# Kernel optimization log

Measured on AMD Instinct MI355X. Metric: run time of the kernel, lower is better.

Reference implementation:

```python
import jax, jax.numpy as jnp
import numpy as np

N = 16384       # num_nodes
IN = 128        # in_features
OUT = 128       # out_features
E = 524288      # num edges
NG = 8          # FastKAN num_grids
GRID_MIN, GRID_MAX = -2.0, 2.0
LN_EPS = 1e-5


def setup_inputs() -> dict:
    key = jax.random.key(0)
    ks = jax.random.split(key, 6)
    x = jax.random.normal(ks[0], (N, IN), dtype=jnp.float32)
    edge_index = jax.random.randint(ks[1], (2, E), 0, N, dtype=jnp.int32)
    # FastKANLayer params
    ln_gamma = jnp.ones((IN,), jnp.float32)
    ln_beta = jnp.zeros((IN,), jnp.float32)
    # SplineLinear: trunc-normal-ish init with scale 0.1 (fast-kan default)
    spline_w = (jax.random.normal(ks[2], (OUT, IN * NG), jnp.float32)
                * (0.1 / np.sqrt(IN * NG)))
    base_w = jax.random.normal(ks[3], (OUT, IN), jnp.float32) / np.sqrt(IN)
    base_b = jnp.zeros((OUT,), jnp.float32)
    # GCNConv.bias
    bias = jax.random.normal(ks[4], (OUT,), jnp.float32) * 0.01
    return dict(x=x, edge_index=edge_index, ln_gamma=ln_gamma, ln_beta=ln_beta,
                spline_w=spline_w, base_w=base_w, base_b=base_b, bias=bias)


def _fastkan(x, ln_gamma, ln_beta, spline_w, base_w, base_b):
    # LayerNorm
    mu = jnp.mean(x, axis=-1, keepdims=True)
    var = jnp.mean((x - mu) ** 2, axis=-1, keepdims=True)
    h = (x - mu) * jax.lax.rsqrt(var + LN_EPS) * ln_gamma + ln_beta
    # Gaussian RBF basis over fixed grid
    grid = jnp.linspace(GRID_MIN, GRID_MAX, NG)
    denom = (GRID_MAX - GRID_MIN) / (NG - 1)
    basis = jnp.exp(-(((h[..., None] - grid) / denom) ** 2))  # [N, IN, NG]
    out = basis.reshape(x.shape[0], IN * NG) @ spline_w.T      # [N, OUT]
    out = out + jax.nn.silu(x) @ base_w.T + base_b             # base update
    return out


def reference(x, edge_index, ln_gamma, ln_beta, spline_w, base_w, base_b, bias):
    num_nodes = x.shape[0]
    # Dense symmetric adjacency, exactly as the torch module builds it
    adj = jnp.zeros((num_nodes, num_nodes), x.dtype)
    adj = adj.at[edge_index[0], edge_index[1]].set(1.0)
    adj = adj.at[edge_index[1], edge_index[0]].set(1.0)
    deg = jnp.sum(adj, axis=1)
    dis = 1.0 / jnp.sqrt(deg)
    norm_adj = adj * dis[:, None] * dis[None, :]
    support = _fastkan(x, ln_gamma, ln_beta, spline_w, base_w, base_b)
    return norm_adj @ support + bias
```

## Files before the change

kernel.cpp:

```cpp
#include <hip/hip_runtime.h>

#define N_NODES 16384
#define NE 524288
#define KDIM 1152
#define KPH 576
#define KPAD2 584
#define KSTEPS_PH 18
#define NBUCK 1024
#define SBLK 512
#define SPB 2048
#define MROW 516
#define DCAP 256

typedef unsigned int uint32;
typedef unsigned short ushort;
typedef __attribute__((ext_vector_type(8))) short bf16x8;
typedef __attribute__((ext_vector_type(4))) float f32x4;

__device__ __forceinline__ ushort f2bf(float f) {
    unsigned u = __float_as_uint(f);
    unsigned r = (u + 0x7fffu + ((u >> 16) & 1u)) >> 16;
    return (ushort)r;
}
__device__ __forceinline__ float bflo(uint32 u) {
    return __uint_as_float(u << 16);
}
__device__ __forceinline__ float bfhi(uint32 u) {
    return __uint_as_float(u & 0xffff0000u);
}

__global__ __launch_bounds__(256) void pre_kernel(
    const int* __restrict__ ei, uint32* __restrict__ ebuf,
    uint32* __restrict__ ocnt, const float* __restrict__ sw,
    const float* __restrict__ bw, ushort* __restrict__ Wp) {
    const int t = threadIdx.x;
    if (blockIdx.x >= SBLK) {
        int idx = (blockIdx.x - SBLK) * 256 + t;
        int i  = idx & 7;
        int l  = (idx >> 3) & 63;
        int ct = (idx >> 9) & 7;
        int kk = idx >> 12;
        int kp  = kk * 32 + ((l >> 4) << 3) + i;
        int p   = kp / KPH;
        int r   = kp - p * KPH;
        int col = ct * 16 + (l & 15);
        float v;
        if (r < 512) {
            int ch = p * 64 + (r >> 3);
            int g  = r & 7;
            v = sw[col * 1024 + ch * 8 + g];
        } else {
            int ch = p * 64 + (r - 512);
            v = bw[col * 128 + ch];
        }
        Wp[idx] = f2bf(v);
        return;
    }
    __shared__ int hcnt[NBUCK];
    __shared__ int lbase[NBUCK];
    __shared__ int ps[256];
    __shared__ uint32 st[SPB];
    for (int q = t; q < NBUCK; q += 256) hcnt[q] = 0;
    __syncthreads();

    int bk[8], sl[8];
    uint32 pk[8];
#pragma unroll
    for (int k = 0; k < 4; ++k) {
        int e = blockIdx.x * 1024 + k * 256 + t;
        int a = ei[e];
        int b = ei[NE + e];
        bk[2 * k]     = a >> 4;
        pk[2 * k]     = ((uint32)(a & 15) << 14) | (uint32)b;
        bk[2 * k + 1] = b >> 4;
        pk[2 * k + 1] = ((uint32)(b & 15) << 14) | (uint32)a;
        sl[2 * k]     = atomicAdd(&hcnt[bk[2 * k]], 1);
        sl[2 * k + 1] = atomicAdd(&hcnt[bk[2 * k + 1]], 1);
    }
    __syncthreads();

    int c[4], loc[4];
    int s = 0;
#pragma unroll
    for (int q = 0; q < 4; ++q) {
        c[q] = hcnt[t * 4 + q];
        loc[q] = s;
        s += c[q];
    }
    ps[t] = s;
    __syncthreads();
    for (int off = 1; off < 256; off <<= 1) {
        int v = ps[t];
        int add = (t >= off) ? ps[t - off] : 0;
        __syncthreads();
        ps[t] = v + add;
        __syncthreads();
    }
    const int base = (t == 0) ? 0 : ps[t - 1];
    uint32* oc = ocnt + (size_t)blockIdx.x * NBUCK;
#pragma unroll
    for (int q = 0; q < 4; ++q) {
        int e0 = base + loc[q];
        lbase[t * 4 + q] = e0;
        oc[t * 4 + q] = (uint32)e0 | ((uint32)c[q] << 16);
    }
    __syncthreads();

#pragma unroll
    for (int k = 0; k < 8; ++k) st[lbase[bk[k]] + sl[k]] = pk[k];
    __syncthreads();
    uint32* gout = ebuf + (size_t)blockIdx.x * SPB;
#pragma unroll
    for (int k = 0; k < 8; ++k) gout[t + k * 256] = st[t + k * 256];
}

__global__ __launch_bounds__(256) void mid_kernel(
    const uint32* __restrict__ ebuf, const uint32* __restrict__ ocnt,
    float* __restrict__ dis, int* __restrict__ degarr,
    ushort* __restrict__ dadj, const float* __restrict__ x,
    const float* __restrict__ gamma, const float* __restrict__ beta,
    const ushort* __restrict__ Wp, const float* __restrict__ base_b,
    ushort* __restrict__ S) {
    __shared__ __align__(16) ushort smem[32 * KPAD2];
    const int t = threadIdx.x;
    const int lane = t & 63;
    const int w = t >> 6;
    const int role = blockIdx.x % 3;

    if (role < 2) {
        uint32* mask = (uint32*)smem;
        const int bkt = (blockIdx.x / 3) * 2 + role;
        for (int i = t; i < 16 * MROW; i += 256) mask[i] = 0;
        __syncthreads();

        const uint32 oc0 = ocnt[(size_t)t * NBUCK + bkt];
        const uint32 oc1 = ocnt[(size_t)(t + 256) * NBUCK + bkt];
#pragma unroll
        for (int h = 0; h < 2; ++h) {
            const int b = h ? (t + 256) : t;
            const uint32 oc = h ? oc1 : oc0;
            int off = (int)(oc & 0xFFFFu);
            int cn  = (int)(oc >> 16);
            const uint32* p = ebuf + (size_t)b * SPB + off;
            for (int s = 0; s < cn; ++s) {
                uint32 e = p[s];
                atomicOr(&mask[(e >> 14) * MROW + ((e & 16383) >> 5)],
                         1u << (e & 31));
            }
        }
        __syncthreads();

        for (int n = w * 4; n < w * 4 + 4; ++n) {
            const uint32* row = &mask[n * MROW];
            uint32 wd[8];
            int c = 0;
#pragma unroll
            for (int j = 0; j < 8; ++j) {
                wd[j] = row[lane + 64 * j];
                c += __popc(wd[j]);
            }
            int inc = c;
#pragma unroll
            for (int o = 1; o < 64; o <<= 1) {
                int v = __shfl_up(inc, o);
                if (lane >= o) inc += v;
            }
            int total = __shfl(inc, 63);
            int pos = inc - c;
            const int node = bkt * 16 + n;
            if (lane == 0) {
                dis[node] = rsqrtf((float)total);
                degarr[node] = total > DCAP ? DCAP : total;
            }
            ushort* drow = dadj + (size_t)node * DCAP;
#pragma unroll
            for (int j = 0; j < 8; ++j) {
                uint32 bits = wd[j];
                int base = (lane + 64 * j) * 32;
                while (bits) {
                    int b = __ffs(bits) - 1;
                    bits &= bits - 1;
                    if (pos < DCAP) drow[pos] = (ushort)(base + b);
                    ++pos;
                }
            }
        }
        return;
    }

    ushort* Bs = smem;
    const int nodeBase = (blockIdx.x / 3) * 32;

    const float g0 = gamma[lane], g1 = gamma[lane + 64];
    const float be0 = beta[lane], be1 = beta[lane + 64];

    float h0r[8], h1r[8], f0r[8], f1r[8];
#pragma unroll
    for (int j = 0; j < 8; ++j) {
        const int row = nodeBase + w * 8 + j;
        float f0 = x[(size_t)row * 128 + lane];
        float f1 = x[(size_t)row * 128 + lane + 64];
        float s = f0 + f1;
#pragma unroll
        for (int o = 32; o; o >>= 1) s += __shfl_xor(s, o);
        float mu = s * 0.0078125f;
        float d0 = f0 - mu, d1 = f1 - mu;
        float v = d0 * d0 + d1 * d1;
#pragma unroll
        for (int o = 32; o; o >>= 1) v += __shfl_xor(v, o);
        float rstd = rsqrtf(v * 0.0078125f + 1e-5f);
        h0r[j] = d0 * rstd * g0 + be0;
        h1r[j] = d1 * rstd * g1 + be1;
        f0r[j] = f0;
        f1r[j] = f1;
    }

    const int ct0 = w * 2;
    f32x4 accA = {0.f, 0.f, 0.f, 0.f};
    f32x4 accB = {0.f, 0.f, 0.f, 0.f};
    f32x4 accC = {0.f, 0.f, 0.f, 0.f};
    f32x4 accD = {0.f, 0.f, 0.f, 0.f};
    const ushort* Alo = &Bs[(lane & 15) * KPAD2 + (lane >> 4) * 8];
    const ushort* Ahi = Alo + 16 * KPAD2;
    const bf16x8* Wv = (const bf16x8*)Wp;

#pragma unroll
    for (int p = 0; p < 2; ++p) {
        if (p) __syncthreads();
#pragma unroll
        for (int j = 0; j < 8; ++j) {
            const int n = w * 8 + j;
            const float h = p ? h1r[j] : h0r[j];
            const float f = p ? f1r[j] : f0r[j];
            ushort pk[8] __attribute__((aligned(16)));
#pragma unroll
            for (int g = 0; g < 8; ++g) {
                float gv = -2.0f + (float)g * (4.0f / 7.0f);
                float z = (h - gv) * 1.75f;
                pk[g] = f2bf(__expf(-z * z));
            }
            *reinterpret_cast<uint4*>(&Bs[n * KPAD2 + lane * 8]) =
                *reinterpret_cast<const uint4*>(pk);
            Bs[n * KPAD2 + 512 + lane] = f2bf(f / (1.0f + __expf(-f)));
        }
        __syncthreads();

#pragma unroll 3
        for (int kkl = 0; kkl < KSTEPS_PH; ++kkl) {
            const int kkg = p * KSTEPS_PH + kkl;
            bf16x8 alo = *reinterpret_cast<const bf16x8*>(Alo + kkl * 32);
            bf16x8 ahi = *reinterpret_cast<const bf16x8*>(Ahi + kkl * 32);
            bf16x8 b0 = Wv[(size_t)(kkg * 8 + ct0) * 64 + lane];
            bf16x8 b1 = Wv[(size_t)(kkg * 8 + ct0 + 1) * 64 + lane];
            accA = __builtin_amdgcn_mfma_f32_16x16x32_bf16(alo, b0, accA, 0, 0, 0);
            accB = __builtin_amdgcn_mfma_f32_16x16x32_bf16(alo, b1, accB, 0, 0, 0);
            accC = __builtin_amdgcn_mfma_f32_16x16x32_bf16(ahi, b0, accC, 0, 0, 0);
            accD = __builtin_amdgcn_mfma_f32_16x16x32_bf16(ahi, b1, accD, 0, 0, 0);
        }
    }

    const int col0 = ct0 * 16 + (lane & 15);
    const int rbase = (lane >> 4) * 4;
    const float bb0 = base_b[col0];
    const float bb1 = base_b[col0 + 16];
#pragma unroll
    for (int r = 0; r < 4; ++r) {
        const int rlo = nodeBase + rbase + r;
        const int rhi = rlo + 16;
        S[(size_t)rlo * 128 + col0]      = f2bf(accA[r] + bb0);
        S[(size_t)rlo * 128 + col0 + 16] = f2bf(accB[r] + bb1);
        S[(size_t)rhi * 128 + col0]      = f2bf(accC[r] + bb0);
        S[(size_t)rhi * 128 + col0 + 16] = f2bf(accD[r] + bb1);
    }
}

__global__ __launch_bounds__(256) void aggregate_kernel(
    const int* __restrict__ degarr, const ushort* __restrict__ dadj,
    const ushort* __restrict__ S, const float* __restrict__ dis,
    const float* __restrict__ bias, float* __restrict__ out) {
    __shared__ ushort lst[2][DCAP];
    __shared__ float part[2][2][128];
    const int t = threadIdx.x;
    const int g = t >> 7;
    const int tl = t & 127;
    const int i = blockIdx.x * 2 + g;

    const int total = degarr[i];
    const ushort* drow = dadj + (size_t)i * DCAP;
    if (tl < total) lst[g][tl] = drow[tl];
    if (tl + 128 < total) lst[g][tl + 128] = drow[tl + 128];
    __syncthreads();

    const int lane = t & 63;
    const int wv = (t >> 6) & 1;
    const int slot = lane >> 4;
    const int cl = lane & 15;
    const uint4* S128 = (const uint4*)S;
    float acc[8] = {0.f, 0.f, 0.f, 0.f, 0.f, 0.f, 0.f, 0.f};

    for (int base = wv * 4; base < total; base += 16) {
        const int ia = base + slot;
        const int ib = base + 8 + slot;
        const int ja = lst[g][ia < total ? ia : (total - 1)];
        const int jb = lst[g][ib < total ? ib : (total - 1)];
        const float da = (ia < total) ? dis[ja] : 0.0f;
        const float db = (ib < total) ? dis[jb] : 0.0f;
        const uint4 ua = S128[(size_t)ja * 16 + cl];
        const uint4 ub = S128[(size_t)jb * 16 + cl];
        acc[0] += da * bflo(ua.x) + db * bflo(ub.x);
        acc[1] += da * bfhi(ua.x) + db * bfhi(ub.x);
        acc[2] += da * bflo(ua.y) + db * bflo(ub.y);
        acc[3] += da * bfhi(ua.y) + db * bfhi(ub.y);
        acc[4] += da * bflo(ua.z) + db * bflo(ub.z);
        acc[5] += da * bfhi(ua.z) + db * bfhi(ub.z);
        acc[6] += da * bflo(ua.w) + db * bflo(ub.w);
        acc[7] += da * bfhi(ua.w) + db * bfhi(ub.w);
    }

#pragma unroll
    for (int e = 0; e < 8; ++e) {
        acc[e] += __shfl_xor(acc[e], 16);
        acc[e] += __shfl_xor(acc[e], 32);
    }
    if (lane < 16) {
        float4 v0 = {acc[0], acc[1], acc[2], acc[3]};
        float4 v1 = {acc[4], acc[5], acc[6], acc[7]};
        *reinterpret_cast<float4*>(&part[g][wv][cl * 8])     = v0;
        *reinterpret_cast<float4*>(&part[g][wv][cl * 8 + 4]) = v1;
    }
    __syncthreads();

    float v = part[g][0][tl] + part[g][1][tl];
    out[(size_t)i * 128 + tl] = v * dis[i] + bias[tl];
}

extern "C" void kernel_launch(void* const* d_in, const int* in_sizes, int n_in,
                              void* d_out, int out_size, void* d_ws, size_t ws_size,
                              hipStream_t stream) {
    const float* x        = (const float*)d_in[0];
    const int*   ei       = (const int*)d_in[1];
    const float* ln_gamma = (const float*)d_in[2];
    const float* ln_beta  = (const float*)d_in[3];
    const float* spline_w = (const float*)d_in[4];
    const float* base_w   = (const float*)d_in[5];
    const float* base_b   = (const float*)d_in[6];
    const float* bias     = (const float*)d_in[7];
    float* out = (float*)d_out;

    char* ws = (char*)d_ws;
    const size_t WP_OFF   = 0;
    const size_t DIS_OFF  = 294912;
    const size_t DEG_OFF  = 360448;
    const size_t DADJ_OFF = 425984;
    const size_t OCNT_OFF = 8814592;
    const size_t EBUF_OFF = 10911744;
    const size_t S_OFF    = 15106048;
    const size_t NEEDED   = 19300352;
    if (ws_size < NEEDED) return;

    ushort* Wp     = (ushort*)(ws + WP_OFF);
    float*  dis    = (float*)(ws + DIS_OFF);
    int*    degarr = (int*)(ws + DEG_OFF);
    ushort* dadj   = (ushort*)(ws + DADJ_OFF);
    uint32* ocnt   = (uint32*)(ws + OCNT_OFF);
    uint32* ebuf   = (uint32*)(ws + EBUF_OFF);
    ushort* S      = (ushort*)(ws + S_OFF);

    pre_kernel<<<SBLK + 576, 256, 0, stream>>>(ei, ebuf, ocnt,
                                               spline_w, base_w, Wp);
    mid_kernel<<<1536, 256, 0, stream>>>(ebuf, ocnt, dis, degarr, dadj,
                                         x, ln_gamma, ln_beta, Wp, base_b, S);
    aggregate_kernel<<<N_NODES / 2, 256, 0, stream>>>(degarr, dadj, S, dis,
                                                      bias, out);
}
```

Before: 66.01 us.

## Split aggregation into two column-half passes for L2 locality of S gathers

The neighbour list of each node is partitioned by neighbour index into a low half (nodes below 8192) and a high half, with the low-half count packed into the degree array. The aggregation kernel now runs twice: the first pass gathers only low-half neighbours and writes partial sums, and the second gathers high-half neighbours, adds the partial, then applies normalisation and bias. Each pass touches only half of the support matrix S, which is meant to raise cache hit rates on the random gathers. The cost is an extra kernel launch, an extra read and write of the output, and a second scan per row in mid_kernel.

Measured after the change: 76.13 us. +15.3%, slower.

```diff
diff --git a/kernel.cpp b/kernel.cpp
--- a/kernel.cpp
+++ b/kernel.cpp
@@ -153,28 +153,55 @@
         for (int n = w * 4; n < w * 4 + 4; ++n) {
             const uint32* row = &mask[n * MROW];
             uint32 wd[8];
-            int c = 0;
-#pragma unroll
-            for (int j = 0; j < 8; ++j) {
+            int cL = 0, cH = 0;
+#pragma unroll
+            for (int j = 0; j < 4; ++j) {
                 wd[j] = row[lane + 64 * j];
-                c += __popc(wd[j]);
-            }
-            int inc = c;
+                cL += __popc(wd[j]);
+            }
+#pragma unroll
+            for (int j = 4; j < 8; ++j) {
+                wd[j] = row[lane + 64 * j];
+                cH += __popc(wd[j]);
+            }
+            int incL = cL;
 #pragma unroll
             for (int o = 1; o < 64; o <<= 1) {
-                int v = __shfl_up(inc, o);
-                if (lane >= o) inc += v;
-            }
-            int total = __shfl(inc, 63);
-            int pos = inc - c;
+                int v = __shfl_up(incL, o);
+                if (lane >= o) incL += v;
+            }
+            const int totalL = __shfl(incL, 63);
+            int incH = cH;
+#pragma unroll
+            for (int o = 1; o < 64; o <<= 1) {
+                int v = __shfl_up(incH, o);
+                if (lane >= o) incH += v;
+            }
+            const int totalH = __shfl(incH, 63);
+            const int total = totalL + totalH;
             const int node = bkt * 16 + n;
             if (lane == 0) {
                 dis[node] = rsqrtf((float)total);
-                degarr[node] = total > DCAP ? DCAP : total;
+                int dcl = total > DCAP ? DCAP : total;
+                int lcl = totalL > DCAP ? DCAP : totalL;
+                degarr[node] = dcl | (lcl << 16);
             }
             ushort* drow = dadj + (size_t)node * DCAP;
-#pragma unroll
-            for (int j = 0; j < 8; ++j) {
+            int pos = incL - cL;
+#pragma unroll
+            for (int j = 0; j < 4; ++j) {
+                uint32 bits = wd[j];
+                int base = (lane + 64 * j) * 32;
+                while (bits) {
+                    int b = __ffs(bits) - 1;
+                    bits &= bits - 1;
+                    if (pos < DCAP) drow[pos] = (ushort)(base + b);
+                    ++pos;
+                }
+            }
+            pos = totalL + incH - cH;
+#pragma unroll
+            for (int j = 4; j < 8; ++j) {
                 uint32 bits = wd[j];
                 int base = (lane + 64 * j) * 32;
                 while (bits) {
@@ -275,9 +302,10 @@
 }
 
 __global__ __launch_bounds__(256) void aggregate_kernel(
-    const int* __restrict__ degarr, const ushort* __restrict__ dadj,
-    const ushort* __restrict__ S, const float* __restrict__ dis,
-    const float* __restrict__ bias, float* __restrict__ out) {
+    const int pass, const int* __restrict__ degarr,
+    const ushort* __restrict__ dadj, const ushort* __restrict__ S,
+    const float* __restrict__ dis, const float* __restrict__ bias,
+    float* __restrict__ out) {
     __shared__ ushort lst[2][DCAP];
     __shared__ float part[2][2][128];
     const int t = threadIdx.x;
@@ -285,8 +313,12 @@
     const int tl = t & 127;
     const int i = blockIdx.x * 2 + g;
 
-    const int total = degarr[i];
-    const ushort* drow = dadj + (size_t)i * DCAP;
+    const int dp = degarr[i];
+    const int deg = dp & 0xFFFF;
+    const int cLow = dp >> 16;
+    const int lo = pass ? cLow : 0;
+    const int total = pass ? (deg - cLow) : cLow;
+    const ushort* drow = dadj + (size_t)i * DCAP + lo;
     if (tl < total) lst[g][tl] = drow[tl];
     if (tl + 128 < total) lst[g][tl + 128] = drow[tl + 128];
     __syncthreads();
@@ -331,7 +363,11 @@
     __syncthreads();
 
     float v = part[g][0][tl] + part[g][1][tl];
-    out[(size_t)i * 128 + tl] = v * dis[i] + bias[tl];
+    if (pass == 0)
+        out[(size_t)i * 128 + tl] = v;
+    else
+        out[(size_t)i * 128 + tl] =
+            (out[(size_t)i * 128 + tl] + v) * dis[i] + bias[tl];
 }
 
 extern "C" void kernel_launch(void* const* d_in, const int* in_sizes, int n_in,
@@ -370,6 +406,8 @@
                                                spline_w, base_w, Wp);
     mid_kernel<<<1536, 256, 0, stream>>>(ebuf, ocnt, dis, degarr, dadj,
                                          x, ln_gamma, ln_beta, Wp, base_b, S);
-    aggregate_kernel<<<N_NODES / 2, 256, 0, stream>>>(degarr, dadj, S, dis,
+    aggregate_kernel<<<N_NODES / 2, 256, 0, stream>>>(0, degarr, dadj, S, dis,
                                                       bias, out);
-}
+    aggregate_kernel<<<N_NODES / 2, 256, 0, stream>>>(1, degarr, dadj, S, dis,
+                                                      bias, out);
+}
```
